# Optimization experiments

Hardware: AMD Instinct MI355X
Metric: run time of the kernel (lower is better)

## Reference

```python
import jax, jax.numpy as jnp
import numpy as np
from jax import lax

DIM = 96; HEADS = 3; WS = 8; SS = 4; HRES = 256; WRES = 256
HD = DIM // HEADS; SCALE = HD ** -0.5; N = WS * WS


def _rel_pos():
    # signed-log relative coordinates, [N, N, 2]
    c = np.arange(WS)
    coords = np.stack(np.meshgrid(c, c, indexing='ij')).reshape(2, -1)
    rel = (coords[:, :, None] - coords[:, None, :]).transpose(1, 2, 0).astype(np.float32)
    return np.sign(rel) * np.log1p(np.abs(rel))


def _attn_mask():
    # Swin-style shift mask, [nW, N, N] with 0 / -100
    img = np.zeros((HRES, WRES), np.float32)
    sl = (slice(0, -WS), slice(-WS, -SS), slice(-SS, None))
    cnt = 0
    for hs in sl:
        for ws in sl:
            img[hs, ws] = cnt
            cnt += 1
    mw = img.reshape(HRES // WS, WS, WRES // WS, WS).transpose(0, 2, 1, 3).reshape(-1, N)
    d = mw[:, None, :] - mw[:, :, None]
    return np.where(d != 0, -100.0, 0.0).astype(np.float32)

REL = jnp.asarray(_rel_pos())
MASK = jnp.asarray(_attn_mask())


def _conv1x1(x, w, b):
    return jnp.einsum('oc,bchw->bohw', w, x) + b[None, :, None, None]


def setup_inputs() -> dict:
    key = jax.random.key(0)
    ks = jax.random.split(key, 14)
    f = lambda k, s, sc=0.02: jax.random.normal(k, s, jnp.float32) * sc
    return {
        'x':   jax.random.normal(ks[0], (4, DIM, HRES, WRES), jnp.float32),
        'Wv':  f(ks[1], (DIM, DIM)),       'bv':  f(ks[2], (DIM,)),
        'Wqk': f(ks[3], (2 * DIM, DIM)),   'bqk': f(ks[4], (2 * DIM,)),
        'Wm1': f(ks[5], (2, 256), 0.1),    'bm1': f(ks[6], (256,)),
        'Wm2': f(ks[7], (256, HEADS), 0.1),'bm2': f(ks[8], (HEADS,)),
        'Wdw': f(ks[9], (DIM, 1, 5, 5)),   'bdw': f(ks[10], (DIM,)),
        'Wp':  f(ks[11], (DIM, DIM)),      'bp':  f(ks[12], (DIM,)),
    }


def reference(x, Wv, bv, Wqk, bqk, Wm1, bm1, Wm2, bm2, Wdw, bdw, Wp, bp):
    B, C, H, W = x.shape
    V = _conv1x1(x, Wv, bv)                      # [B,C,H,W]
    QK = _conv1x1(x, Wqk, bqk)                   # [B,2C,H,W]
    qkv = jnp.concatenate([QK, V], axis=1).transpose(0, 2, 3, 1)  # [B,H,W,3C]
    qkv = jnp.roll(qkv, (-SS, -SS), axis=(1, 2))
    nh, nw = H // WS, W // WS
    win = qkv.reshape(B, nh, WS, nw, WS, 3 * C).transpose(0, 1, 3, 2, 4, 5)
    win = win.reshape(B * nh * nw, N, 3 * C)     # [B_, N, 3C]
    q, k, v = [t.reshape(-1, N, HEADS, HD).transpose(0, 2, 1, 3)
               for t in jnp.split(win, 3, axis=-1)]
    attn = jnp.einsum('bhnd,bhmd->bhnm', q * SCALE, k)           # [B_,h,N,N]
    bias = jax.nn.relu(REL @ Wm1 + bm1) @ Wm2 + bm2              # [N,N,h]
    attn = attn + bias.transpose(2, 0, 1)[None]
    attn = attn.reshape(B, nh * nw, HEADS, N, N) + MASK[None, :, None]
    attn = jax.nn.softmax(attn.reshape(-1, HEADS, N, N), axis=-1)
    out = jnp.einsum('bhnm,bhmd->bnhd', attn, v).reshape(-1, N, C)
    out = out.reshape(B, nh, nw, WS, WS, C).transpose(0, 1, 3, 2, 4, 5).reshape(B, H, W, C)
    out = jnp.roll(out, (SS, SS), axis=(1, 2)).transpose(0, 3, 1, 2)  # [B,C,H,W]
    Vp = jnp.pad(V, ((0, 0), (0, 0), (2, 2), (2, 2)), mode='reflect')
    conv = lax.conv_general_dilated(Vp, Wdw, (1, 1), 'VALID',
                                    feature_group_count=C,
                                    dimension_numbers=('NCHW', 'OIHW', 'NCHW'))
    conv = conv + bdw[None, :, None, None]
    return _conv1x1(conv + out, Wp, bp)
```

## Files before the change

kernel.cpp:

```cpp
#include <hip/hip_runtime.h>
#include <hip/hip_bf16.h>
#include <hip/hip_fp16.h>

#define NHEADS 3
#define SSH 4
#define NWD 32
#define PXI 65536
#define SCALE 0.17677669529663687f

typedef _Float16 f16x8 __attribute__((ext_vector_type(8)));
typedef float f32x4 __attribute__((ext_vector_type(4)));

__global__ __launch_bounds__(256) void k0_wt(
    const float* __restrict__ Wqk, const float* __restrict__ Wv,
    const float* __restrict__ Wp, float* __restrict__ WT,
    float* __restrict__ WTp) {
  int i = blockIdx.x * 256 + threadIdx.x;
  if (i < 288 * 96) {
    int c = i % 96, oc = i / 96;
    float w = (oc < 192) ? Wqk[oc * 96 + c] : Wv[(oc - 192) * 96 + c];
    WT[c * 288 + oc] = w;
  }
  if (i < 96 * 96) {
    int c = i % 96, oc = i / 96;
    WTp[c * 96 + oc] = Wp[oc * 96 + c];
  }
}

__global__ __launch_bounds__(256) void k1_qkv(
    const float* __restrict__ x, const float* __restrict__ WT,
    const float* __restrict__ bqk, const float* __restrict__ bv,
    __half* __restrict__ qkv_h, float* __restrict__ v_b, int b) {
  __shared__ __align__(16) float Xt[96 * 64];
  const int tid = threadIdx.x;
  const int pt = blockIdx.x, ot = blockIdx.y;
  const int p0 = pt * 64;

  for (int i = tid; i < 96 * 16; i += 256) {
    int c = i >> 4, f = i & 15;
    *(float4*)&Xt[c * 64 + f * 4] =
        *(const float4*)&x[(size_t)(b * 96 + c) * PXI + p0 + f * 4];
  }
  __syncthreads();

  const int lane = tid & 63;
  const int wvu = __builtin_amdgcn_readfirstlane(tid >> 6);
  const int oc0l = wvu * 24;
  const int oc0 = ot * 96 + oc0l;

  float acc[24];
#pragma unroll
  for (int r = 0; r < 24; r++) acc[r] = 0.f;

  const float* wt = WT + oc0;
#pragma unroll 4
  for (int c = 0; c < 96; c++) {
    float xa = Xt[c * 64 + lane];
    const float* wc = wt + c * 288;
#pragma unroll
    for (int r = 0; r < 24; r++) acc[r] += wc[r] * xa;
  }

#pragma unroll
  for (int r = 0; r < 24; r++) {
    int oc = oc0 + r;
    acc[r] += (oc < 192) ? bqk[oc] : bv[oc - 192];
  }

  {
    int p = p0 + lane;
    int h = p >> 8, w = p & 255;
    int hp = (h + 252) & 255, wp = (w + 252) & 255;
    int win = (hp >> 3) * NWD + (wp >> 3);
    int n = (hp & 7) * 8 + (wp & 7);

    __align__(16) __half2 hv[12];
#pragma unroll
    for (int r = 0; r < 12; r++)
      hv[r] = __floats2half2_rn(acc[2 * r], acc[2 * r + 1]);
    __half* dst = qkv_h + (size_t)(win * 64 + n) * 288 + oc0;
    const float4* hv4 = (const float4*)hv;
    *(float4*)&dst[0]  = hv4[0];
    *(float4*)&dst[8]  = hv4[1];
    *(float4*)&dst[16] = hv4[2];

    if (ot == 2) {
#pragma unroll
      for (int r = 0; r < 24; r++)
        v_b[(size_t)(oc0l + r) * PXI + p] = acc[r];
    }
  }
}

__global__ __launch_bounds__(256) void k2_bias(
    const float* __restrict__ Wm1, const float* __restrict__ bm1,
    const float* __restrict__ Wm2, const float* __restrict__ bm2,
    float* __restrict__ bias_c) {
  int pair = blockIdx.x * 256 + threadIdx.x;
  int n = pair >> 6, m = pair & 63;
  float d0 = (float)((n >> 3) - (m >> 3));
  float d1 = (float)((n & 7) - (m & 7));
  float r0 = (d0 > 0.f ? 1.f : (d0 < 0.f ? -1.f : 0.f)) * log1pf(fabsf(d0));
  float r1 = (d1 > 0.f ? 1.f : (d1 < 0.f ? -1.f : 0.f)) * log1pf(fabsf(d1));
  float a0 = 0.f, a1 = 0.f, a2 = 0.f;
  for (int j = 0; j < 256; j++) {
    float hb = r0 * Wm1[j] + r1 * Wm1[256 + j] + bm1[j];
    hb = fmaxf(hb, 0.f);
    a0 += hb * Wm2[j * 3 + 0];
    a1 += hb * Wm2[j * 3 + 1];
    a2 += hb * Wm2[j * 3 + 2];
  }
  int ti = n >> 4, g = (n >> 2) & 3, reg = n & 3;
  int tj = m >> 4, c = m & 15;
  int lane = (g << 4) | c;
  int idx = lane * 64 + (ti * 4 + tj) * 4 + reg;
  bias_c[0 * 4096 + idx] = a0 + bm2[0];
  bias_c[1 * 4096 + idx] = a1 + bm2[1];
  bias_c[2 * 4096 + idx] = a2 + bm2[2];
}

__global__ __launch_bounds__(64) void k3_attn(
    const __half* __restrict__ qkv_h, const float* __restrict__ bias_c,
    float* __restrict__ o_b) {
  __shared__ _Float16 P_lds[64 * 72];
  const int lane = threadIdx.x;
  const int g = lane >> 4;
  const int c = lane & 15;
  const int win = blockIdx.x;
  const int hd = blockIdx.y;
  const int wh = win >> 5, ww = win & 31;

  const __half* qb = qkv_h + (size_t)win * 64 * 288 + hd * 32;

  f16x8 qf[4], kf[4];
#pragma unroll
  for (int t = 0; t < 4; t++) {
    qf[t] = *(const f16x8*)(const void*)&qb[(size_t)(16 * t + c) * 288 + 8 * g];
    kf[t] = *(const f16x8*)(const void*)&qb[(size_t)(16 * t + c) * 288 + 96 + 8 * g];
  }
#pragma unroll
  for (int t = 0; t < 4; t++)
#pragma unroll
    for (int e = 0; e < 8; e++) qf[t][e] *= (_Float16)SCALE;

  f32x4 S[4][4];
  {
    const float* bc = bias_c + (size_t)hd * 4096 + lane * 64;
#pragma unroll
    for (int ti = 0; ti < 4; ti++)
#pragma unroll
      for (int tj = 0; tj < 4; tj++)
        S[ti][tj] = *(const f32x4*)&bc[(ti * 4 + tj) * 4];
  }

  if (wh == 31 || ww == 31) {
#pragma unroll
    for (int ti = 0; ti < 4; ti++)
#pragma unroll
      for (int r = 0; r < 4; r++) {
        int row = 16 * ti + 4 * g + r;
        int rn = ((wh == 31) ? (((row >> 3) < 4) ? 1 : 2) : 0) * 3 +
                 ((ww == 31) ? (((row & 7) < 4) ? 1 : 2) : 0);
#pragma unroll
        for (int tj = 0; tj < 4; tj++) {
          int m = 16 * tj + c;
          int rm = ((wh == 31) ? (((m >> 3) < 4) ? 1 : 2) : 0) * 3 +
                   ((ww == 31) ? (((m & 7) < 4) ? 1 : 2) : 0);
          if (rm != rn) S[ti][tj][r] -= 100.f;
        }
      }
  }

#pragma unroll
  for (int tn = 0; tn < 4; tn++)
#pragma unroll
    for (int tm = 0; tm < 4; tm++)
      S[tn][tm] = __builtin_amdgcn_mfma_f32_16x16x32_f16(qf[tn], kf[tm],
                                                         S[tn][tm], 0, 0, 0);

  const __half* vbse = qb + 192;
  f16x8 vf[2][2];
#pragma unroll
  for (int td = 0; td < 2; td++)
#pragma unroll
    for (int km = 0; km < 2; km++) {
      f16x8 v = {};
#pragma unroll
      for (int i = 0; i < 8; i++)
        v[i] = *(const _Float16*)&vbse[(size_t)(32 * km + 8 * g + i) * 288 +
                                       16 * td + c];
      vf[td][km] = v;
    }

#pragma unroll
  for (int ti = 0; ti < 4; ti++)
#pragma unroll
    for (int tj = 0; tj < 4; tj++)
#pragma unroll
      for (int r = 0; r < 4; r++) S[ti][tj][r] = __expf(S[ti][tj][r]);

  float invs[4][4];
#pragma unroll
  for (int ti = 0; ti < 4; ti++)
#pragma unroll
    for (int r = 0; r < 4; r++) {
      float sm = (S[ti][0][r] + S[ti][1][r]) + (S[ti][2][r] + S[ti][3][r]);
      sm += __shfl_xor(sm, 1);
      sm += __shfl_xor(sm, 2);
      sm += __shfl_xor(sm, 4);
      sm += __shfl_xor(sm, 8);
      invs[ti][r] = 1.f / sm;
    }

  {
    const int cx = (4 * g) & 8;
#pragma unroll
    for (int ti = 0; ti < 4; ti++)
#pragma unroll
      for (int r = 0; r < 4; r++) {
        int row = 16 * ti + 4 * g + r;
        int rx = (4 * g + r) & 8;
#pragma unroll
        for (int tj = 0; tj < 4; tj++)
          P_lds[row * 72 + ((16 * tj + c) ^ rx)] = (_Float16)S[ti][tj][r];
      }
    (void)cx;
  }

  f32x4 O[4][2];
#pragma unroll
  for (int tn = 0; tn < 4; tn++) {
    const int row = 16 * tn + c;
    const int rx = c & 8;
    f16x8 pf0 = *(const f16x8*)(const void*)&P_lds[row * 72 + ((8 * g) ^ rx)];
    f16x8 pf1 = *(const f16x8*)(const void*)&P_lds[row * 72 + ((32 + 8 * g) ^ rx)];
#pragma unroll
    for (int td = 0; td < 2; td++) {
      f32x4 oo = {0.f, 0.f, 0.f, 0.f};
      oo = __builtin_amdgcn_mfma_f32_16x16x32_f16(pf0, vf[td][0], oo, 0, 0, 0);
      oo = __builtin_amdgcn_mfma_f32_16x16x32_f16(pf1, vf[td][1], oo, 0, 0, 0);
      O[tn][td] = oo;
    }
  }

#pragma unroll
  for (int tn = 0; tn < 4; tn++)
#pragma unroll
    for (int r = 0; r < 4; r++) {
      int row = 16 * tn + 4 * g + r;
      int hpix = ((wh << 3) + (row >> 3) + SSH) & 255;
      int wpix = ((ww << 3) + (row & 7) + SSH) & 255;
      size_t pix = (size_t)(hpix << 8) + wpix;
      float inv = invs[tn][r];
#pragma unroll
      for (int td = 0; td < 2; td++) {
        int cch = hd * 32 + 16 * td + c;
        o_b[(size_t)cch * PXI + pix] = O[tn][td][r] * inv;
      }
    }
}

__global__ __launch_bounds__(256) void k4_dw(
    const float* __restrict__ v_b, const float* __restrict__ o_b,
    const float* __restrict__ Wdw, const float* __restrict__ bdw,
    float* __restrict__ t_b) {
  const int blk = blockIdx.x;
  const int c = blk >> 8;
  const int h = blk & 255;
  const int w = threadIdx.x;
  __shared__ float wd[25];
  __shared__ float bd;
  if (threadIdx.x < 25) wd[threadIdx.x] = Wdw[c * 25 + threadIdx.x];
  if (threadIdx.x == 32) bd = bdw[c];
  __syncthreads();

  const float* vp = v_b + ((size_t)c << 16);
  float acc = bd;
#pragma unroll
  for (int dy = 0; dy < 5; dy++) {
    int hh = h + dy - 2;
    hh = hh < 0 ? -hh : (hh > 255 ? 510 - hh : hh);
    const float* row = vp + (hh << 8);
#pragma unroll
    for (int dx = 0; dx < 5; dx++) {
      int wx = w + dx - 2;
      wx = wx < 0 ? -wx : (wx > 255 ? 510 - wx : wx);
      acc += row[wx] * wd[dy * 5 + dx];
    }
  }
  size_t idx = ((size_t)c << 16) + (h << 8) + w;
  acc += o_b[idx];
  t_b[idx] = acc;
}

__global__ __launch_bounds__(256) void k5_proj(
    const float* __restrict__ t_b, const float* __restrict__ WTp,
    const float* __restrict__ bp, float* __restrict__ out, int b) {
  __shared__ __align__(16) float Xt[96 * 64];
  const int tid = threadIdx.x;
  const int pt = blockIdx.x;
  const int p0 = pt * 64;

  for (int i = tid; i < 96 * 16; i += 256) {
    int c = i >> 4, f = i & 15;
    *(float4*)&Xt[c * 64 + f * 4] =
        *(const float4*)&t_b[(size_t)c * PXI + p0 + f * 4];
  }
  __syncthreads();

  const int lane = tid & 63;
  const int wvu = __builtin_amdgcn_readfirstlane(tid >> 6);
  const int oc0 = wvu * 24;

  float acc[24];
#pragma unroll
  for (int r = 0; r < 24; r++) acc[r] = 0.f;

  const float* wt = WTp + oc0;
#pragma unroll 4
  for (int c = 0; c < 96; c++) {
    float xa = Xt[c * 64 + lane];
    const float* wc = wt + c * 96;
#pragma unroll
    for (int r = 0; r < 24; r++) acc[r] += wc[r] * xa;
  }

  int p = p0 + lane;
#pragma unroll
  for (int r = 0; r < 24; r++) {
    int oc = oc0 + r;
    out[(size_t)(b * 96 + oc) * PXI + p] = acc[r] + bp[oc];
  }
}

extern "C" void kernel_launch(void* const* d_in, const int* in_sizes, int n_in,
                              void* d_out, int out_size, void* d_ws,
                              size_t ws_size, hipStream_t stream) {
  const float* x   = (const float*)d_in[0];
  const float* Wv  = (const float*)d_in[1];
  const float* bv  = (const float*)d_in[2];
  const float* Wqk = (const float*)d_in[3];
  const float* bqk = (const float*)d_in[4];
  const float* Wm1 = (const float*)d_in[5];
  const float* bm1 = (const float*)d_in[6];
  const float* Wm2 = (const float*)d_in[7];
  const float* bm2 = (const float*)d_in[8];
  const float* Wdw = (const float*)d_in[9];
  const float* bdw = (const float*)d_in[10];
  const float* Wp  = (const float*)d_in[11];
  const float* bp  = (const float*)d_in[12];

  char* ws = (char*)d_ws;
  __half* qkv_h = (__half*)ws;
  float* t_b   = (float*)ws;
  float* v_b   = (float*)(ws + 37748736);
  float* o_b   = (float*)(ws + 62914560);
  float* bias_c = (float*)(ws + 88080384);
  float* WT    = (float*)(ws + 88129536);
  float* WTp   = (float*)(ws + 88240128);

  k0_wt<<<108, 256, 0, stream>>>(Wqk, Wv, Wp, WT, WTp);
  k2_bias<<<16, 256, 0, stream>>>(Wm1, bm1, Wm2, bm2, bias_c);
  for (int b = 0; b < 4; b++) {
    k1_qkv<<<dim3(1024, 3), 256, 0, stream>>>(x, WT, bqk, bv, qkv_h, v_b, b);
    k3_attn<<<dim3(1024, 3), 64, 0, stream>>>(qkv_h, bias_c, o_b);
    k4_dw<<<24576, 256, 0, stream>>>(v_b, o_b, Wdw, bdw, t_b);
    k5_proj<<<1024, 256, 0, stream>>>(t_b, WTp, bp, (float*)d_out, b);
  }
}
```

Measured before the change: 712.5 us.

## Compute QKV projection with fp16 MFMA using hi/lo split of inputs

Replaces the scalar FP32 QKV 1x1-conv kernel with an MFMA 16x16x32 f16 implementation. Weights are pre-converted to fp16, and x is split into high and low fp16 parts so the fp32 inputs keep extra precision. Each block now covers all 288 output channels for 64 pixels, so x is read once instead of three times and the LDS staging goes away. The risks are reduced precision from the fp16 weights and strided global loads of x without LDS.

```diff
diff --git a/kernel.cpp b/kernel.cpp
--- a/kernel.cpp
+++ b/kernel.cpp
@@ -13,81 +13,72 @@
 
 __global__ __launch_bounds__(256) void k0_wt(
     const float* __restrict__ Wqk, const float* __restrict__ Wv,
-    const float* __restrict__ Wp, float* __restrict__ WT,
-    float* __restrict__ WTp) {
+    const float* __restrict__ Wp, const float* __restrict__ bqk,
+    const float* __restrict__ bv, _Float16* __restrict__ WHh,
+    float* __restrict__ WTp, float* __restrict__ bias288) {
   int i = blockIdx.x * 256 + threadIdx.x;
   if (i < 288 * 96) {
     int c = i % 96, oc = i / 96;
     float w = (oc < 192) ? Wqk[oc * 96 + c] : Wv[(oc - 192) * 96 + c];
-    WT[c * 288 + oc] = w;
+    WHh[oc * 96 + c] = (_Float16)w;
   }
   if (i < 96 * 96) {
     int c = i % 96, oc = i / 96;
     WTp[c * 96 + oc] = Wp[oc * 96 + c];
   }
+  if (i < 288) bias288[i] = (i < 192) ? bqk[i] : bv[i - 192];
 }
 
 __global__ __launch_bounds__(256) void k1_qkv(
-    const float* __restrict__ x, const float* __restrict__ WT,
-    const float* __restrict__ bqk, const float* __restrict__ bv,
-    __half* __restrict__ qkv_h, float* __restrict__ v_b, int b) {
-  __shared__ __align__(16) float Xt[96 * 64];
+    const float* __restrict__ x, const _Float16* __restrict__ WHh,
+    const float* __restrict__ bias288, __half* __restrict__ qkv_h,
+    float* __restrict__ v_b, int b) {
   const int tid = threadIdx.x;
-  const int pt = blockIdx.x, ot = blockIdx.y;
-  const int p0 = pt * 64;
-
-  for (int i = tid; i < 96 * 16; i += 256) {
-    int c = i >> 4, f = i & 15;
-    *(float4*)&Xt[c * 64 + f * 4] =
-        *(const float4*)&x[(size_t)(b * 96 + c) * PXI + p0 + f * 4];
-  }
-  __syncthreads();
-
   const int lane = tid & 63;
-  const int wvu = __builtin_amdgcn_readfirstlane(tid >> 6);
-  const int oc0l = wvu * 24;
-  const int oc0 = ot * 96 + oc0l;
-
-  float acc[24];
-#pragma unroll
-  for (int r = 0; r < 24; r++) acc[r] = 0.f;
-
-  const float* wt = WT + oc0;
-#pragma unroll 4
-  for (int c = 0; c < 96; c++) {
-    float xa = Xt[c * 64 + lane];
-    const float* wc = wt + c * 288;
-#pragma unroll
-    for (int r = 0; r < 24; r++) acc[r] += wc[r] * xa;
-  }
-
-#pragma unroll
-  for (int r = 0; r < 24; r++) {
-    int oc = oc0 + r;
-    acc[r] += (oc < 192) ? bqk[oc] : bv[oc - 192];
-  }
-
-  {
-    int p = p0 + lane;
-    int h = p >> 8, w = p & 255;
-    int hp = (h + 252) & 255, wp = (w + 252) & 255;
-    int win = (hp >> 3) * NWD + (wp >> 3);
-    int n = (hp & 7) * 8 + (wp & 7);
-
-    __align__(16) __half2 hv[12];
-#pragma unroll
-    for (int r = 0; r < 12; r++)
-      hv[r] = __floats2half2_rn(acc[2 * r], acc[2 * r + 1]);
-    __half* dst = qkv_h + (size_t)(win * 64 + n) * 288 + oc0;
-    const float4* hv4 = (const float4*)hv;
-    *(float4*)&dst[0]  = hv4[0];
-    *(float4*)&dst[8]  = hv4[1];
-    *(float4*)&dst[16] = hv4[2];
-
-    if (ot == 2) {
-#pragma unroll
-      for (int r = 0; r < 24; r++)
-        v_b[(size_t)(oc0l + r) * PXI + p] = acc[r];
+  const int wv = tid >> 6;
+  const int g = lane >> 4, c = lane & 15;
+  const int px = blockIdx.x * 64 + wv * 16 + c;
+
+  const float* xb = x + (size_t)b * 96 * PXI + px;
+  f16x8 xh[3], xl[3];
+#pragma unroll
+  for (int kb = 0; kb < 3; kb++) {
+    float xv[8];
+#pragma unroll
+    for (int i = 0; i < 8; i++)
+      xv[i] = xb[(size_t)(32 * kb + 8 * g + i) * PXI];
+#pragma unroll
+    for (int i = 0; i < 8; i++) {
+      _Float16 h = (_Float16)xv[i];
+      xh[kb][i] = h;
+      xl[kb][i] = (_Float16)(xv[i] - (float)h);
+    }
+  }
+
+  const int hq = px >> 8, wq = px & 255;
+  const int hp = (hq + 252) & 255, wp = (wq + 252) & 255;
+  const int win = (hp >> 3) * NWD + (wp >> 3);
+  const int n = (hp & 7) * 8 + (wp & 7);
+  __half* qdst = qkv_h + (size_t)(win * 64 + n) * 288;
+
+#pragma unroll 3
+  for (int tm = 0; tm < 18; tm++) {
+    f32x4 acc = *(const f32x4*)&bias288[16 * tm + 4 * g];
+#pragma unroll
+    for (int kb = 0; kb < 3; kb++) {
+      f16x8 a = *(const f16x8*)&WHh[(size_t)(16 * tm + c) * 96 + 32 * kb + 8 * g];
+      acc = __builtin_amdgcn_mfma_f32_16x16x32_f16(a, xh[kb], acc, 0, 0, 0);
+      acc = __builtin_amdgcn_mfma_f32_16x16x32_f16(a, xl[kb], acc, 0, 0, 0);
+    }
+    __align__(8) __half2 hv[2];
+    hv[0] = __floats2half2_rn(acc[0], acc[1]);
+    hv[1] = __floats2half2_rn(acc[2], acc[3]);
+    *(float2*)&qdst[16 * tm + 4 * g] = *(const float2*)hv;
+    if (tm >= 12) {
+      int oc = 16 * tm + 4 * g - 192;
+#pragma unroll
+      for (int r = 0; r < 4; r++)
+        v_b[(size_t)(oc + r) * PXI + px] = acc[r];
     }
   }
 }
@@ -213,7 +204,6 @@
     }
 
   {
-    const int cx = (4 * g) & 8;
 #pragma unroll
     for (int ti = 0; ti < 4; ti++)
 #pragma unroll
@@ -224,7 +214,6 @@
         for (int tj = 0; tj < 4; tj++)
           P_lds[row * 72 + ((16 * tj + c) ^ rx)] = (_Float16)S[ti][tj][r];
       }
-    (void)cx;
   }
 
   f32x4 O[4][2];
@@ -356,13 +345,14 @@
   float* v_b   = (float*)(ws + 37748736);
   float* o_b   = (float*)(ws + 62914560);
   float* bias_c = (float*)(ws + 88080384);
-  float* WT    = (float*)(ws + 88129536);
-  float* WTp   = (float*)(ws + 88240128);
-
-  k0_wt<<<108, 256, 0, stream>>>(Wqk, Wv, Wp, WT, WTp);
+  float* WTp   = (float*)(ws + 88129536);
+  _Float16* WHh = (_Float16*)(ws + 88166400);
+  float* bias288 = (float*)(ws + 88221696);
+
+  k0_wt<<<108, 256, 0, stream>>>(Wqk, Wv, Wp, bqk, bv, WHh, WTp, bias288);
   k2_bias<<<16, 256, 0, stream>>>(Wm1, bm1, Wm2, bm2, bias_c);
   for (int b = 0; b < 4; b++) {
-    k1_qkv<<<dim3(1024, 3), 256, 0, stream>>>(x, WT, bqk, bv, qkv_h, v_b, b);
+    k1_qkv<<<1024, 256, 0, stream>>>(x, WHh, bias288, qkv_h, v_b, b);
     k3_attn<<<dim3(1024, 3), 64, 0, stream>>>(qkv_h, bias_c, o_b);
     k4_dw<<<24576, 256, 0, stream>>>(v_b, o_b, Wdw, bdw, t_b);
     k5_proj<<<1024, 256, 0, stream>>>(t_b, WTp, bp, (float*)d_out, b);
```

Measured after the change: 629.9 us. 11.6% less time.
